# Kernel tuning notes

Hardware: AMD Instinct MI355X
Metric: run time of the kernel (lower is better)

The kernel has to match this reference:

```python
import jax, jax.numpy as jnp
import numpy as np

N_NODES = 50000
N_EDGES = 800000
NFEAT = 96
NHID = 128
EPS = 1e-12  # F.normalize default eps


def setup_inputs() -> dict:
    key = jax.random.key(0)
    k1, k2, k3, k4 = jax.random.split(key, 4)
    edge_index = jax.random.randint(k1, (2, N_EDGES), 0, N_NODES, dtype=jnp.int64)
    x = jax.random.normal(k2, (N_NODES, NFEAT), dtype=jnp.float32)
    # Glorot-ish scaling for linear weights
    W_l = jax.random.normal(k3, (NHID, NFEAT), dtype=jnp.float32) * (1.0 / np.sqrt(NFEAT))
    b_l = jnp.zeros((NHID,), dtype=jnp.float32)
    W_r = jax.random.normal(k4, (NHID, NFEAT), dtype=jnp.float32) * (1.0 / np.sqrt(NFEAT))
    return {"edge_index": edge_index, "x": x, "W_l": W_l, "b_l": b_l, "W_r": W_r}


def reference(edge_index, x, W_l, b_l, W_r):
    # PyG SAGEConv, aggr='mean', root_weight=True, normalize=True
    src, dst = edge_index[0], edge_index[1]
    # gather source features, scatter-sum into destination nodes
    msg_sum = jax.ops.segment_sum(x[src], dst, num_segments=N_NODES)  # [N, nfeat]
    deg = jax.ops.segment_sum(jnp.ones((edge_index.shape[1],), dtype=x.dtype),
                              dst, num_segments=N_NODES)
    agg = msg_sum / jnp.maximum(deg, 1.0)[:, None]  # mean; isolated nodes -> 0
    out = agg @ W_l.T + b_l + x @ W_r.T  # [N, nhid]
    # L2 normalize per node (F.normalize p=2, dim=-1)
    norm = jnp.linalg.norm(out, axis=-1, keepdims=True)
    return out / jnp.maximum(norm, EPS)
```

## Files before the change

### kernel.cpp

```cpp
#include <hip/hip_runtime.h>


typedef __attribute__((ext_vector_type(8))) short short8;
typedef __attribute__((ext_vector_type(4))) float floatx4;
typedef __attribute__((ext_vector_type(2))) float floatx2;

constexpr int kNodes = 50000;
constexpr int kEdges = 800000;
constexpr int kF = 96;
constexpr int kH = 128;
constexpr int kEllW = 32;
constexpr int kSpillCap = 4096;
constexpr int kBktRange = kNodes / 8;
constexpr int kCurStride = 16;
constexpr int kChunksP = 782;
constexpr int kStgCap = 192;

constexpr size_t kXhOff    = 0;
constexpr size_t kXqOff    = 9600000;
constexpr size_t kStgOff   = 14400000;
constexpr size_t kWhOff    = 19204608;
constexpr size_t kEllOff   = 19253760;
constexpr size_t kCurOff   = 22453760;
constexpr size_t kSpcOff   = 25653760;
constexpr size_t kSpillOff = 25653776;
constexpr size_t kCntOff   = 25670160;

constexpr int kMega2Blocks = kChunksP * 4;
constexpr int kPrepBlocks  = kChunksP * 3;
constexpr int kPrepItems   = kNodes * kF / 8 + kH * 192 / 8;
constexpr int kPrepStride  = kPrepBlocks * 256;

constexpr int kRowS = 104;

__device__ __forceinline__ unsigned pack2_bf16(float a, float b) {
  unsigned ua = __float_as_uint(a), ub = __float_as_uint(b);
  ua = (ua + 0x7fffu + ((ua >> 16) & 1u)) >> 16;
  ub = (ub + 0x7fffu + ((ub >> 16) & 1u)) >> 16;
  return ua | (ub << 16);
}

__device__ __forceinline__ void acc8_fp8(const uint2 v, float* a) {
  floatx2 f;
  f = __builtin_amdgcn_cvt_pk_f32_fp8((int)v.x, false); a[0] += f.x; a[1] += f.y;
  f = __builtin_amdgcn_cvt_pk_f32_fp8((int)v.x, true);  a[2] += f.x; a[3] += f.y;
  f = __builtin_amdgcn_cvt_pk_f32_fp8((int)v.y, false); a[4] += f.x; a[5] += f.y;
  f = __builtin_amdgcn_cvt_pk_f32_fp8((int)v.y, true);  a[6] += f.x; a[7] += f.y;
}

__device__ __forceinline__ void ell_insert(int dst, int src, int* cursor,
                                           ushort* ell, unsigned* spill,
                                           int* spillCnt) {
  const int slot = atomicAdd(&cursor[(size_t)dst * kCurStride], 1);
  if (slot < kEllW) {
    ell[(size_t)dst * kEllW + ((slot & 3) << 3) + (slot >> 2)] = (ushort)src;
  } else {
    const int sp = atomicAdd(spillCnt, 1);
    if (sp < kSpillCap) spill[sp] = ((unsigned)dst << 16) | (unsigned)src;
  }
}

__global__ void __launch_bounds__(256)
mega2_kernel(const int* __restrict__ ei, const float* __restrict__ x,
             const float* __restrict__ Wl, const float* __restrict__ Wr,
             uint4* __restrict__ xh4, uint2* __restrict__ xq2,
             uint4* __restrict__ wh4, unsigned* __restrict__ stg,
             int* __restrict__ cnt, int* __restrict__ cursor,
             unsigned* __restrict__ spill, int* __restrict__ spillCnt) {
  const int p = blockIdx.x >> 2;
  const int r = blockIdx.x & 3;
  if (r == 0) {
    const int zi = p * 256 + threadIdx.x;
    if (zi < 200000) reinterpret_cast<uint4*>(cursor)[zi] = make_uint4(0, 0, 0, 0);
    if (zi == 0) *spillCnt = 0;
    __shared__ int lcnt[8];
    if (threadIdx.x < 8) lcnt[threadIdx.x] = 0;
    __syncthreads();
    const int base = p * 1024 + threadIdx.x;
    int d[4], s[4];
#pragma unroll
    for (int k = 0; k < 4; ++k) {
      const int e = base + k * 256;
      const bool v = e < kEdges;
      d[k] = v ? ei[kEdges + e] : -1;
      s[k] = v ? ei[e] : 0;
    }
#pragma unroll
    for (int k = 0; k < 4; ++k) {
      if (d[k] >= 0) {
        const int b = d[k] / kBktRange;
        const int pos = atomicAdd(&lcnt[b], 1);
        if (pos < kStgCap) {
          stg[((size_t)p * 8 + b) * kStgCap + pos] =
              ((unsigned)d[k] << 16) | (unsigned)s[k];
        } else {
          const int sp = atomicAdd(spillCnt, 1);
          if (sp < kSpillCap)
            spill[sp] = ((unsigned)d[k] << 16) | (unsigned)s[k];
        }
      }
    }
    __syncthreads();
    if (threadIdx.x < 8)
      cnt[p * 8 + threadIdx.x] = min(lcnt[threadIdx.x], kStgCap);
    return;
  }
  constexpr int kCvt = kNodes * kF / 8;
  const int pid = p * 3 + (r - 1);
  for (int i = pid * 256 + threadIdx.x; i < kPrepItems; i += kPrepStride) {
    if (i < kCvt) {
      const float4 v0 = reinterpret_cast<const float4*>(x)[i * 2];
      const float4 v1 = reinterpret_cast<const float4*>(x)[i * 2 + 1];
      uint4 o;
      o.x = pack2_bf16(v0.x, v0.y);
      o.y = pack2_bf16(v0.z, v0.w);
      o.z = pack2_bf16(v1.x, v1.y);
      o.w = pack2_bf16(v1.z, v1.w);
      xh4[i] = o;
      int u0 = __builtin_amdgcn_cvt_pk_fp8_f32(v0.x, v0.y, 0, false);
      u0 = __builtin_amdgcn_cvt_pk_fp8_f32(v0.z, v0.w, u0, true);
      int u1 = __builtin_amdgcn_cvt_pk_fp8_f32(v1.x, v1.y, 0, false);
      u1 = __builtin_amdgcn_cvt_pk_fp8_f32(v1.z, v1.w, u1, true);
      xq2[i] = make_uint2((unsigned)u0, (unsigned)u1);
    } else {
      const int j = i - kCvt;
      const int row = j / 24, chunk = j % 24;
      const float* src = (chunk < 12) ? (Wl + (size_t)row * kF + chunk * 8)
                                      : (Wr + (size_t)row * kF + (chunk - 12) * 8);
      const float4 v0 = reinterpret_cast<const float4*>(src)[0];
      const float4 v1 = reinterpret_cast<const float4*>(src)[1];
      uint4 o;
      o.x = pack2_bf16(v0.x, v0.y);
      o.y = pack2_bf16(v0.z, v0.w);
      o.z = pack2_bf16(v1.x, v1.y);
      o.w = pack2_bf16(v1.z, v1.w);
      wh4[j] = o;
    }
  }
}

__global__ void __launch_bounds__(256)
fillp_kernel(const unsigned* __restrict__ stg, const int* __restrict__ cnt,
             int* __restrict__ cursor, ushort* __restrict__ ell,
             unsigned* __restrict__ spill, int* __restrict__ spillCnt) {
  const int g = blockIdx.x & 7;
  for (int chunk = blockIdx.x >> 3; chunk < kChunksP; chunk += gridDim.x >> 3) {
    const int n = cnt[chunk * 8 + g];
    const unsigned* reg = stg + ((size_t)chunk * 8 + g) * kStgCap;
    for (int i = threadIdx.x; i < n; i += 256) {
      const unsigned pr = reg[i];
      ell_insert((int)(pr >> 16), (int)(pr & 0xffffu), cursor, ell, spill,
                 spillCnt);
    }
  }
}

__global__ void __launch_bounds__(256)
gm_kernel(const uint2* __restrict__ xq2, const uint4* __restrict__ xh4,
          const int* __restrict__ cursor, const ushort* __restrict__ ell,
          const unsigned* __restrict__ spill, const int* __restrict__ spillCnt,
          const uint4* __restrict__ wh4, const float* __restrict__ bl,
          float* __restrict__ out) {
  __shared__ __align__(16) short sAgg[16 * kRowS];
  __shared__ float sP[4][4][4];

  const int wave = threadIdx.x >> 6, lane = threadIdx.x & 63;
  const int g = blockIdx.x & 7;
  const int j = blockIdx.x >> 3;
  const int tstart = (g * 3125) >> 3;
  const int tend = ((g + 1) * 3125) >> 3;
  const int tile = tstart + j;
  if (tile >= tend) return;
  const int base = tile * 16;

  const int slot = lane / 12;
  const int c = lane % 12;
  const bool gactive = lane < 48;
  const int slotc = gactive ? slot : 0;
  const int sc = min(*spillCnt, kSpillCap);

#pragma unroll
  for (int it = 0; it < 2; ++it) {
    const int nA = base + wave * 4 + it * 2;
    const int nB = nA + 1;
    const int degA = cursor[(size_t)nA * kCurStride];
    const int degB = cursor[(size_t)nB * kCurStride];
    const int dmA = min(degA, kEllW);
    const int dmB = min(degB, kEllW);

    const uint4 ivA = *reinterpret_cast<const uint4*>(
        ell + (size_t)nA * kEllW + (slotc << 3));
    const uint4 ivB = *reinterpret_cast<const uint4*>(
        ell + (size_t)nB * kEllW + (slotc << 3));
    const unsigned wa[4] = {ivA.x, ivA.y, ivA.z, ivA.w};
    const unsigned wb[4] = {ivB.x, ivB.y, ivB.z, ivB.w};

    float a[8] = {0.f, 0.f, 0.f, 0.f, 0.f, 0.f, 0.f, 0.f};
    float b[8] = {0.f, 0.f, 0.f, 0.f, 0.f, 0.f, 0.f, 0.f};

#pragma unroll
    for (int k = 0; k < 8; ++k) {
      const int idx = (k << 2) + slot;
      const int srcA = (k & 1) ? (int)(wa[k >> 1] >> 16) : (int)(wa[k >> 1] & 0xffffu);
      const int srcB = (k & 1) ? (int)(wb[k >> 1] >> 16) : (int)(wb[k >> 1] & 0xffffu);
      if (gactive && idx < dmA) acc8_fp8(xq2[(size_t)srcA * 12 + c], a);
      if (gactive && idx < dmB) acc8_fp8(xq2[(size_t)srcB * 12 + c], b);
    }
    for (int jj = 0; jj < sc; ++jj) {
      const unsigned pr = spill[jj];
      const int pd = (int)(pr >> 16);
      if (lane < 12 && (pd == nA || pd == nB)) {
        const uint2 v = xq2[(size_t)(pr & 0xffffu) * 12 + c];
        if (pd == nA) acc8_fp8(v, a); else acc8_fp8(v, b);
      }
    }
#pragma unroll
    for (int f = 0; f < 8; ++f) {
      a[f] += __shfl(a[f], lane + 24, 64);
      b[f] += __shfl(b[f], lane + 24, 64);
    }
#pragma unroll
    for (int f = 0; f < 8; ++f) {
      a[f] += __shfl(a[f], lane + 12, 64);
      b[f] += __shfl(b[f], lane + 12, 64);
    }

    if (lane < 12) {
      const float invA = 1.0f / fmaxf((float)degA, 1.0f);
      uint4 o;
      o.x = pack2_bf16(a[0] * invA, a[1] * invA);
      o.y = pack2_bf16(a[2] * invA, a[3] * invA);
      o.z = pack2_bf16(a[4] * invA, a[5] * invA);
      o.w = pack2_bf16(a[6] * invA, a[7] * invA);
      *reinterpret_cast<uint4*>(&sAgg[(wave * 4 + it * 2) * kRowS + c * 8]) = o;
      const float invB = 1.0f / fmaxf((float)degB, 1.0f);
      uint4 p;
      p.x = pack2_bf16(b[0] * invB, b[1] * invB);
      p.y = pack2_bf16(b[2] * invB, b[3] * invB);
      p.z = pack2_bf16(b[4] * invB, b[5] * invB);
      p.w = pack2_bf16(b[6] * invB, b[7] * invB);
      *reinterpret_cast<uint4*>(&sAgg[(wave * 4 + it * 2 + 1) * kRowS + c * 8]) = p;
    }
  }
  __syncthreads();

  const int r = lane & 15, q = lane >> 4;
  const int cg0 = wave * 2;
  const short8* xhS = reinterpret_cast<const short8*>(xh4);
  const short8* whS = reinterpret_cast<const short8*>(wh4);

  floatx4 fac[2] = {};
#pragma unroll
  for (int ks = 0; ks < 6; ++ks) {
    short8 a;
    if (ks < 3) {
      a = *reinterpret_cast<const short8*>(&sAgg[r * kRowS + (ks * 4 + q) * 8]);
    } else {
      a = xhS[(size_t)(base + r) * 12 + (ks - 3) * 4 + q];
    }
#pragma unroll
    for (int i = 0; i < 2; ++i) {
      const short8 b = whS[((cg0 + i) * 16 + r) * 24 + ks * 4 + q];
      fac[i] = __builtin_amdgcn_mfma_f32_16x16x32_bf16(a, b, fac[i], 0, 0, 0);
    }
  }

  float p0 = 0.f, p1 = 0.f, p2 = 0.f, p3 = 0.f;
#pragma unroll
  for (int i = 0; i < 2; ++i) {
    const float bb = bl[(cg0 + i) * 16 + r];
    fac[i][0] += bb; fac[i][1] += bb; fac[i][2] += bb; fac[i][3] += bb;
    p0 += fac[i][0] * fac[i][0];
    p1 += fac[i][1] * fac[i][1];
    p2 += fac[i][2] * fac[i][2];
    p3 += fac[i][3] * fac[i][3];
  }
#pragma unroll
  for (int off = 1; off < 16; off <<= 1) {
    p0 += __shfl_xor(p0, off, 64);
    p1 += __shfl_xor(p1, off, 64);
    p2 += __shfl_xor(p2, off, 64);
    p3 += __shfl_xor(p3, off, 64);
  }
  if (r == 0) {
    sP[wave][q][0] = p0; sP[wave][q][1] = p1;
    sP[wave][q][2] = p2; sP[wave][q][3] = p3;
  }
  __syncthreads();
  const float t0 = sP[0][q][0] + sP[1][q][0] + sP[2][q][0] + sP[3][q][0];
  const float t1 = sP[0][q][1] + sP[1][q][1] + sP[2][q][1] + sP[3][q][1];
  const float t2 = sP[0][q][2] + sP[1][q][2] + sP[2][q][2] + sP[3][q][2];
  const float t3 = sP[0][q][3] + sP[1][q][3] + sP[2][q][3] + sP[3][q][3];
  const float s0 = 1.0f / fmaxf(sqrtf(t0), 1e-12f);
  const float s1 = 1.0f / fmaxf(sqrtf(t1), 1e-12f);
  const float s2 = 1.0f / fmaxf(sqrtf(t2), 1e-12f);
  const float s3 = 1.0f / fmaxf(sqrtf(t3), 1e-12f);

#pragma unroll
  for (int i = 0; i < 2; ++i) {
    const int col = (cg0 + i) * 16 + r;
    float* o = out + (size_t)(base + q * 4) * kH + col;
    o[0 * kH] = fac[i][0] * s0;
    o[1 * kH] = fac[i][1] * s1;
    o[2 * kH] = fac[i][2] * s2;
    o[3 * kH] = fac[i][3] * s3;
  }
}

extern "C" void kernel_launch(void* const* d_in, const int* in_sizes, int n_in,
                              void* d_out, int out_size, void* d_ws, size_t ws_size,
                              hipStream_t stream) {
  const int*   ei = (const int*)d_in[0];
  const float* x  = (const float*)d_in[1];
  const float* Wl = (const float*)d_in[2];
  const float* bl = (const float*)d_in[3];
  const float* Wr = (const float*)d_in[4];
  float* out = (float*)d_out;

  char* ws = (char*)d_ws;
  uint4*    xh4      = (uint4*)(ws + kXhOff);
  uint2*    xq2      = (uint2*)(ws + kXqOff);
  unsigned* stg      = (unsigned*)(ws + kStgOff);
  uint4*    wh4      = (uint4*)(ws + kWhOff);
  ushort*   ell      = (ushort*)(ws + kEllOff);
  int*      cursor   = (int*)(ws + kCurOff);
  int*      spillCnt = (int*)(ws + kSpcOff);
  unsigned* spill    = (unsigned*)(ws + kSpillOff);
  int*      cnt      = (int*)(ws + kCntOff);

  mega2_kernel<<<kMega2Blocks, 256, 0, stream>>>(
      ei, x, Wl, Wr, xh4, xq2, wh4, stg, cnt, cursor, spill, spillCnt);

  fillp_kernel<<<3128, 256, 0, stream>>>(stg, cnt, cursor, ell, spill, spillCnt);

  gm_kernel<<<3128, 256, 0, stream>>>(xq2, xh4, cursor, ell, spill, spillCnt,
                                      wh4, bl, out);
}
```

Baseline: 96.50 us.

## Split input conversion between bucketing and ELL-fill kernels to balance load

```diff
diff --git a/kernel.cpp b/kernel.cpp
--- a/kernel.cpp
+++ b/kernel.cpp
@@ -26,10 +26,8 @@
 constexpr size_t kSpillOff = 25653776;
 constexpr size_t kCntOff   = 25670160;
 
-constexpr int kMega2Blocks = kChunksP * 4;
-constexpr int kPrepBlocks  = kChunksP * 3;
-constexpr int kPrepItems   = kNodes * kF / 8 + kH * 192 / 8;
-constexpr int kPrepStride  = kPrepBlocks * 256;
+constexpr int kPrepItems = kNodes * kF / 8 + kH * 192 / 8;
+constexpr int kPrepSplit = 301568;
 
 constexpr int kRowS = 104;
 
@@ -46,6 +44,43 @@
   f = __builtin_amdgcn_cvt_pk_f32_fp8((int)v.x, true);  a[2] += f.x; a[3] += f.y;
   f = __builtin_amdgcn_cvt_pk_f32_fp8((int)v.y, false); a[4] += f.x; a[5] += f.y;
   f = __builtin_amdgcn_cvt_pk_f32_fp8((int)v.y, true);  a[6] += f.x; a[7] += f.y;
+}
+
+__device__ __forceinline__ void prep_item(int i, const float* __restrict__ x,
+                                          const float* __restrict__ Wl,
+                                          const float* __restrict__ Wr,
+                                          uint4* __restrict__ xh4,
+                                          uint2* __restrict__ xq2,
+                                          uint4* __restrict__ wh4) {
+  constexpr int kCvt = kNodes * kF / 8;
+  if (i < kCvt) {
+    const float4 v0 = reinterpret_cast<const float4*>(x)[i * 2];
+    const float4 v1 = reinterpret_cast<const float4*>(x)[i * 2 + 1];
+    uint4 o;
+    o.x = pack2_bf16(v0.x, v0.y);
+    o.y = pack2_bf16(v0.z, v0.w);
+    o.z = pack2_bf16(v1.x, v1.y);
+    o.w = pack2_bf16(v1.z, v1.w);
+    xh4[i] = o;
+    int u0 = __builtin_amdgcn_cvt_pk_fp8_f32(v0.x, v0.y, 0, false);
+    u0 = __builtin_amdgcn_cvt_pk_fp8_f32(v0.z, v0.w, u0, true);
+    int u1 = __builtin_amdgcn_cvt_pk_fp8_f32(v1.x, v1.y, 0, false);
+    u1 = __builtin_amdgcn_cvt_pk_fp8_f32(v1.z, v1.w, u1, true);
+    xq2[i] = make_uint2((unsigned)u0, (unsigned)u1);
+  } else {
+    const int j = i - kCvt;
+    const int row = j / 24, chunk = j % 24;
+    const float* src = (chunk < 12) ? (Wl + (size_t)row * kF + chunk * 8)
+                                    : (Wr + (size_t)row * kF + (chunk - 12) * 8);
+    const float4 v0 = reinterpret_cast<const float4*>(src)[0];
+    const float4 v1 = reinterpret_cast<const float4*>(src)[1];
+    uint4 o;
+    o.x = pack2_bf16(v0.x, v0.y);
+    o.y = pack2_bf16(v0.z, v0.w);
+    o.z = pack2_bf16(v1.x, v1.y);
+    o.w = pack2_bf16(v1.z, v1.w);
+    wh4[j] = o;
+  }
 }
 
 __device__ __forceinline__ void ell_insert(int dst, int src, int* cursor,
@@ -67,9 +102,8 @@
              uint4* __restrict__ wh4, unsigned* __restrict__ stg,
              int* __restrict__ cnt, int* __restrict__ cursor,
              unsigned* __restrict__ spill, int* __restrict__ spillCnt) {
-  const int p = blockIdx.x >> 2;
-  const int r = blockIdx.x & 3;
-  if (r == 0) {
+  const int p = blockIdx.x >> 1;
+  if ((blockIdx.x & 1) == 0) {
     const int zi = p * 256 + threadIdx.x;
     if (zi < 200000) reinterpret_cast<uint4*>(cursor)[zi] = make_uint4(0, 0, 0, 0);
     if (zi == 0) *spillCnt = 0;
@@ -105,54 +139,37 @@
       cnt[p * 8 + threadIdx.x] = min(lcnt[threadIdx.x], kStgCap);
     return;
   }
-  constexpr int kCvt = kNodes * kF / 8;
-  const int pid = p * 3 + (r - 1);
-  for (int i = pid * 256 + threadIdx.x; i < kPrepItems; i += kPrepStride) {
-    if (i < kCvt) {
-      const float4 v0 = reinterpret_cast<const float4*>(x)[i * 2];
-      const float4 v1 = reinterpret_cast<const float4*>(x)[i * 2 + 1];
-      uint4 o;
-      o.x = pack2_bf16(v0.x, v0.y);
-      o.y = pack2_bf16(v0.z, v0.w);
-      o.z = pack2_bf16(v1.x, v1.y);
-      o.w = pack2_bf16(v1.z, v1.w);
-      xh4[i] = o;
-      int u0 = __builtin_amdgcn_cvt_pk_fp8_f32(v0.x, v0.y, 0, false);
-      u0 = __builtin_amdgcn_cvt_pk_fp8_f32(v0.z, v0.w, u0, true);
-      int u1 = __builtin_amdgcn_cvt_pk_fp8_f32(v1.x, v1.y, 0, false);
-      u1 = __builtin_amdgcn_cvt_pk_fp8_f32(v1.z, v1.w, u1, true);
-      xq2[i] = make_uint2((unsigned)u0, (unsigned)u1);
-    } else {
-      const int j = i - kCvt;
-      const int row = j / 24, chunk = j % 24;
-      const float* src = (chunk < 12) ? (Wl + (size_t)row * kF + chunk * 8)
-                                      : (Wr + (size_t)row * kF + (chunk - 12) * 8);
-      const float4 v0 = reinterpret_cast<const float4*>(src)[0];
-      const float4 v1 = reinterpret_cast<const float4*>(src)[1];
-      uint4 o;
-      o.x = pack2_bf16(v0.x, v0.y);
-      o.y = pack2_bf16(v0.z, v0.w);
-      o.z = pack2_bf16(v1.x, v1.y);
-      o.w = pack2_bf16(v1.z, v1.w);
-      wh4[j] = o;
-    }
-  }
+  for (int i = p * 256 + threadIdx.x; i < kPrepSplit; i += kChunksP * 256)
+    prep_item(i, x, Wl, Wr, xh4, xq2, wh4);
 }
 
 __global__ void __launch_bounds__(256)
-fillp_kernel(const unsigned* __restrict__ stg, const int* __restrict__ cnt,
-             int* __restrict__ cursor, ushort* __restrict__ ell,
-             unsigned* __restrict__ spill, int* __restrict__ spillCnt) {
-  const int g = blockIdx.x & 7;
-  for (int chunk = blockIdx.x >> 3; chunk < kChunksP; chunk += gridDim.x >> 3) {
-    const int n = cnt[chunk * 8 + g];
-    const unsigned* reg = stg + ((size_t)chunk * 8 + g) * kStgCap;
-    for (int i = threadIdx.x; i < n; i += 256) {
-      const unsigned pr = reg[i];
-      ell_insert((int)(pr >> 16), (int)(pr & 0xffffu), cursor, ell, spill,
-                 spillCnt);
-    }
-  }
+fillp2_kernel(const unsigned* __restrict__ stg, const int* __restrict__ cnt,
+              int* __restrict__ cursor, ushort* __restrict__ ell,
+              unsigned* __restrict__ spill, int* __restrict__ spillCnt,
+              const float* __restrict__ x, const float* __restrict__ Wl,
+              const float* __restrict__ Wr, uint4* __restrict__ xh4,
+              uint2* __restrict__ xq2, uint4* __restrict__ wh4) {
+  const int q = blockIdx.x >> 4;
+  const int r = blockIdx.x & 15;
+  if (r < 8) {
+    const int g = r;
+#pragma unroll
+    for (int half = 0; half < 2; ++half) {
+      const int chunk = q + half * 391;
+      const int n = cnt[chunk * 8 + g];
+      const unsigned* reg = stg + ((size_t)chunk * 8 + g) * kStgCap;
+      for (int i = threadIdx.x; i < n; i += 256) {
+        const unsigned pr = reg[i];
+        ell_insert((int)(pr >> 16), (int)(pr & 0xffffu), cursor, ell, spill,
+                   spillCnt);
+      }
+    }
+    return;
+  }
+  const int pid = q * 8 + (r - 8);
+  const int i = kPrepSplit + pid * 256 + threadIdx.x;
+  if (i < kPrepItems) prep_item(i, x, Wl, Wr, xh4, xq2, wh4);
 }
 
 __global__ void __launch_bounds__(256)
@@ -244,7 +261,7 @@
   }
   __syncthreads();
 
-  const int r = lane & 15, q = lane >> 4;
+  const int r = lane & 15, q2 = lane >> 4;
   const int cg0 = wave * 2;
   const short8* xhS = reinterpret_cast<const short8*>(xh4);
   const short8* whS = reinterpret_cast<const short8*>(wh4);
@@ -254,13 +271,13 @@
   for (int ks = 0; ks < 6; ++ks) {
     short8 a;
     if (ks < 3) {
-      a = *reinterpret_cast<const short8*>(&sAgg[r * kRowS + (ks * 4 + q) * 8]);
+      a = *reinterpret_cast<const short8*>(&sAgg[r * kRowS + (ks * 4 + q2) * 8]);
     } else {
-      a = xhS[(size_t)(base + r) * 12 + (ks - 3) * 4 + q];
+      a = xhS[(size_t)(base + r) * 12 + (ks - 3) * 4 + q2];
     }
 #pragma unroll
     for (int i = 0; i < 2; ++i) {
-      const short8 b = whS[((cg0 + i) * 16 + r) * 24 + ks * 4 + q];
+      const short8 b = whS[((cg0 + i) * 16 + r) * 24 + ks * 4 + q2];
       fac[i] = __builtin_amdgcn_mfma_f32_16x16x32_bf16(a, b, fac[i], 0, 0, 0);
     }
   }
@@ -283,14 +300,14 @@
     p3 += __shfl_xor(p3, off, 64);
   }
   if (r == 0) {
-    sP[wave][q][0] = p0; sP[wave][q][1] = p1;
-    sP[wave][q][2] = p2; sP[wave][q][3] = p3;
+    sP[wave][q2][0] = p0; sP[wave][q2][1] = p1;
+    sP[wave][q2][2] = p2; sP[wave][q2][3] = p3;
   }
   __syncthreads();
-  const float t0 = sP[0][q][0] + sP[1][q][0] + sP[2][q][0] + sP[3][q][0];
-  const float t1 = sP[0][q][1] + sP[1][q][1] + sP[2][q][1] + sP[3][q][1];
-  const float t2 = sP[0][q][2] + sP[1][q][2] + sP[2][q][2] + sP[3][q][2];
-  const float t3 = sP[0][q][3] + sP[1][q][3] + sP[2][q][3] + sP[3][q][3];
+  const float t0 = sP[0][q2][0] + sP[1][q2][0] + sP[2][q2][0] + sP[3][q2][0];
+  const float t1 = sP[0][q2][1] + sP[1][q2][1] + sP[2][q2][1] + sP[3][q2][1];
+  const float t2 = sP[0][q2][2] + sP[1][q2][2] + sP[2][q2][2] + sP[3][q2][2];
+  const float t3 = sP[0][q2][3] + sP[1][q2][3] + sP[2][q2][3] + sP[3][q2][3];
   const float s0 = 1.0f / fmaxf(sqrtf(t0), 1e-12f);
   const float s1 = 1.0f / fmaxf(sqrtf(t1), 1e-12f);
   const float s2 = 1.0f / fmaxf(sqrtf(t2), 1e-12f);
@@ -299,7 +316,7 @@
 #pragma unroll
   for (int i = 0; i < 2; ++i) {
     const int col = (cg0 + i) * 16 + r;
-    float* o = out + (size_t)(base + q * 4) * kH + col;
+    float* o = out + (size_t)(base + q2 * 4) * kH + col;
     o[0 * kH] = fac[i][0] * s0;
     o[1 * kH] = fac[i][1] * s1;
     o[2 * kH] = fac[i][2] * s2;
@@ -328,10 +345,11 @@
   unsigned* spill    = (unsigned*)(ws + kSpillOff);
   int*      cnt      = (int*)(ws + kCntOff);
 
-  mega2_kernel<<<kMega2Blocks, 256, 0, stream>>>(
+  mega2_kernel<<<kChunksP * 2, 256, 0, stream>>>(
       ei, x, Wl, Wr, xh4, xq2, wh4, stg, cnt, cursor, spill, spillCnt);
 
-  fillp_kernel<<<3128, 256, 0, stream>>>(stg, cnt, cursor, ell, spill, spillCnt);
+  fillp2_kernel<<<391 * 16, 256, 0, stream>>>(
+      stg, cnt, cursor, ell, spill, spillCnt, x, Wl, Wr, xh4, xq2, wh4);
 
   gm_kernel<<<3128, 256, 0, stream>>>(xq2, xh4, cursor, ell, spill, spillCnt,
                                       wh4, bl, out);
```

Result: no change. 95.12 us, median of 2 (-1.4%).
